# Kernel tuning notes

Measured on AMD Instinct MI355X. Metric: run time of the kernel, lower is better.

## Reference

```python
import jax, jax.numpy as jnp
import numpy as np

jax.config.update("jax_enable_x64", True)  # hash uses int64 (prime * coord ~ 7e12)

FEATURE_DIM = 2
GRID_DIM = 3
NUM_LVL = 16
MAX_RES = 2048
MIN_RES = 16
HASH_POWER = 19
MAX_ENTRY = 2 ** HASH_POWER
PRIMES = (3367900313, 2654435761, 805459861)

_b = np.exp((np.log(MAX_RES) - np.log(MIN_RES)) / (NUM_LVL - 1))
RESOLUTIONS = [int(np.floor(MIN_RES * _b ** i)) for i in range(NUM_LVL)]
TABLE_SIZES = [min(r ** GRID_DIM, MAX_ENTRY) for r in RESOLUTIONS]

# Corner offset order matches get_corner(): [c000, c010, c001, c011, c100, c101, c110, c111]
OFFSETS = np.array([[0, 0, 0], [0, 1, 0], [0, 0, 1], [0, 1, 1],
                    [1, 0, 0], [1, 0, 1], [1, 1, 0], [1, 1, 1]], dtype=np.int64)

N = 1 << 20  # number of query points


def setup_inputs() -> dict:
    key = jax.random.key(0)
    kx, kt = jax.random.split(key)
    x = jax.random.uniform(kx, (N, GRID_DIM), dtype=jnp.float32)  # in [0,1]
    # stacked (padded) hashtables; dense levels only use their first res^3 rows
    tables = jax.random.normal(kt, (NUM_LVL, MAX_ENTRY, FEATURE_DIM), dtype=jnp.float32) * 1e-4
    return {"x": x, "tables": tables}


def _level(x, table, res, table_size):
    resf = float(res)
    coord = jnp.clip(x * (resf - 1.0), 0.0, resf - 1.0001)  # [N,3] hash-space coords
    fl = jnp.floor(coord)
    corners = fl.astype(jnp.int64)[:, None, :] + jnp.asarray(OFFSETS)  # [N,8,3]
    if table_size != MAX_ENTRY:
        # dense spatial index: sum_i c_i * res^i
        idx = corners[..., 0] + corners[..., 1] * res + corners[..., 2] * (res * res)
    else:
        # NGP hash: xor of coord*prime, mod table size
        h = (corners[..., 0] * PRIMES[0]) ^ (corners[..., 1] * PRIMES[1]) ^ (corners[..., 2] * PRIMES[2])
        idx = h % MAX_ENTRY
    feat = table[idx]  # [N,8,F] gather
    d = coord - fl  # fractional part, [N,3]
    xx, yy, zz = d[:, 0], d[:, 1], d[:, 2]
    mx, my, mz = 1.0 - xx, 1.0 - yy, 1.0 - zz
    # weight order matches interpolation_weights() stack order
    w = jnp.stack([mx * my * mz, xx * my * mz, mx * yy * mz, xx * yy * mz,
                   mx * my * zz, xx * my * zz, mx * yy * zz, xx * yy * zz], axis=-1)  # [N,8]
    return (feat * w[..., None]).sum(axis=-2)  # [N,F]


def reference(x, tables):
    outs = [_level(x, tables[l], RESOLUTIONS[l], TABLE_SIZES[l]) for l in range(NUM_LVL)]
    return jnp.concatenate(outs, axis=-1)  # [N, NUM_LVL*FEATURE_DIM]
```

## Files before the change

### kernel.cpp

```cpp
#include <hip/hip_runtime.h>
#include <math.h>

#define NLVL 16
#define MAX_ENTRY (1 << 19)
#define NPTS (1 << 20)

typedef float f2_t __attribute__((ext_vector_type(2)));
typedef float f4_t __attribute__((ext_vector_type(4)));

__device__ __forceinline__ void nt_store2(float2 v, float2* p) {
    f2_t t; t.x = v.x; t.y = v.y;
    __builtin_nontemporal_store(t, (f2_t*)p);
}
__device__ __forceinline__ void nt_store4(float4 v, float4* p) {
    f4_t t; t.x = v.x; t.y = v.y; t.z = v.z; t.w = v.w;
    __builtin_nontemporal_store(t, (f4_t*)p);
}
__device__ __forceinline__ float2 nt_load2(const float2* p) {
    f2_t t = __builtin_nontemporal_load((const f2_t*)p);
    return make_float2(t.x, t.y);
}

__device__ __constant__ int OX[8] = {0, 0, 0, 0, 1, 1, 1, 1};
__device__ __constant__ int OY[8] = {0, 1, 0, 1, 0, 0, 1, 1};
__device__ __constant__ int OZ[8] = {0, 0, 1, 1, 0, 1, 0, 1};

__device__ __forceinline__ void corner_setup(
    float x0, float x1, float x2, float s, float hi,
    int& cx, int& cy, int& cz,
    float (&wx)[2], float (&wy)[2], float (&wz)[2])
{
    float c0 = fminf(fmaxf(x0 * s, 0.0f), hi);
    float c1 = fminf(fmaxf(x1 * s, 0.0f), hi);
    float c2 = fminf(fmaxf(x2 * s, 0.0f), hi);
    float f0 = floorf(c0), f1 = floorf(c1), f2 = floorf(c2);
    cx = (int)f0; cy = (int)f1; cz = (int)f2;
    float xx = c0 - f0, yy = c1 - f1, zz = c2 - f2;
    wx[0] = 1.0f - xx; wx[1] = xx;
    wy[0] = 1.0f - yy; wy[1] = yy;
    wz[0] = 1.0f - zz; wz[1] = zz;
}


struct DenseP {
    int res[6];
    int res2[6];
    float scale[6];
    float hi[6];
    long long packoff[6];
    long long nent[6];
};

__global__ __launch_bounds__(256) void repack_kernel(
    const float* __restrict__ tables, float4* __restrict__ pack, DenseP P)
{
    for (int l = 1; l < 6; ++l) {
        const float2* tab = (const float2*)(tables + (size_t)l * MAX_ENTRY * 2);
        float4* dst = pack + P.packoff[l];
        const long long n = P.nent[l];
        for (long long k = blockIdx.x * 256 + threadIdx.x; k < n;
             k += (long long)gridDim.x * 256) {
            const float2 a = tab[k];
            const float2 b = tab[k + 1];
            nt_store4(make_float4(a.x, a.y, b.x, b.y), &dst[k]);
        }
    }
}

__global__ __launch_bounds__(256) void dense_kernel(
    const float* __restrict__ x,
    const float* __restrict__ tables,
    const float4* __restrict__ pack,
    float2* __restrict__ feat,
    DenseP P)
{
    __shared__ float2 lds0[4096];
    {
        const float2* tab0 = (const float2*)tables;
        for (int j = threadIdx.x; j < 4096; j += 256) lds0[j] = tab0[j];
    }
    __syncthreads();

    const int i = blockIdx.x * 256 + threadIdx.x;
    if (i >= NPTS) return;

    const float x0 = x[3 * i + 0];
    const float x1 = x[3 * i + 1];
    const float x2 = x[3 * i + 2];

    {
        int cx, cy, cz;
        float wx[2], wy[2], wz[2];
        corner_setup(x0, x1, x2, P.scale[0], P.hi[0], cx, cy, cz, wx, wy, wz);
        const int res = P.res[0], res2 = P.res2[0];
        const int base = cx + cy * res + cz * res2;
        float a0 = 0.0f, a1 = 0.0f;
#pragma unroll
        for (int k = 0; k < 8; ++k) {
            const int idx = base + OX[k] + OY[k] * res + OZ[k] * res2;
            const float2 f = lds0[idx];
            const float w = wx[k & 1] * wy[(k >> 1) & 1] * wz[k >> 2];
            a0 += w * f.x; a1 += w * f.y;
        }
        nt_store2(make_float2(a0, a1), &feat[i]);
    }

#pragma unroll
    for (int l = 1; l < 6; ++l) {
        int cx, cy, cz;
        float wx[2], wy[2], wz[2];
        corner_setup(x0, x1, x2, P.scale[l], P.hi[l], cx, cy, cz, wx, wy, wz);
        const int res = P.res[l], res2 = P.res2[l];
        const int base = cx + cy * res + cz * res2;
        const float4* pk = pack + P.packoff[l];

        float a0 = 0.0f, a1 = 0.0f;
#pragma unroll
        for (int j = 0; j < 4; ++j) {
            const int idx = base + (j & 1) * res + (j >> 1) * res2;
            const float4 f = pk[idx];
            const float w0 = wx[j & 1] * wy[j >> 1] * wz[0];
            const float w1 = wx[j >> 1] * wy[j & 1] * wz[1];
            a0 += w0 * f.x + w1 * f.z;
            a1 += w0 * f.y + w1 * f.w;
        }
        nt_store2(make_float2(a0, a1), &feat[(size_t)l * NPTS + i]);
    }
}

__device__ __forceinline__ float2 hash_point(
    const float* __restrict__ x, int i, const float2* __restrict__ tab,
    float scale, float hi)
{
    const float x0 = x[3 * i + 0];
    const float x1 = x[3 * i + 1];
    const float x2 = x[3 * i + 2];

    int cx, cy, cz;
    float wx[2], wy[2], wz[2];
    corner_setup(x0, x1, x2, scale, hi, cx, cy, cz, wx, wy, wz);

    const unsigned P0 = 3367900313u, P1 = 2654435761u, P2 = 805459861u;
    unsigned hx[2], hy[2], hz[2];
    hx[0] = (unsigned)cx * P0; hx[1] = hx[0] + P0;
    hy[0] = (unsigned)cy * P1; hy[1] = hy[0] + P1;
    hz[0] = (unsigned)cz * P2; hz[1] = hz[0] + P2;

    float a0 = 0.0f, a1 = 0.0f;
#pragma unroll
    for (int k = 0; k < 8; ++k) {
        const unsigned idx = (hx[OX[k]] ^ hy[OY[k]] ^ hz[OZ[k]]) & (MAX_ENTRY - 1);
        const float2 f = tab[idx];
        const float w = wx[k & 1] * wy[(k >> 1) & 1] * wz[k >> 2];
        a0 += w * f.x; a1 += w * f.y;
    }
    return make_float2(a0, a1);
}

__global__ __launch_bounds__(256) void hash_kernel(
    const float* __restrict__ x,
    const float2* __restrict__ tab,
    float2* __restrict__ featl,
    float scale, float hi)
{
    const int t = blockIdx.x * 256 + threadIdx.x;
    const int i0 = t;
    const int i1 = t + NPTS / 2;
    const float2 r0 = hash_point(x, i0, tab, scale, hi);
    const float2 r1 = hash_point(x, i1, tab, scale, hi);
    nt_store2(r0, &featl[i0]);
    nt_store2(r1, &featl[i1]);
}

__global__ __launch_bounds__(256) void assemble_kernel(
    const float2* __restrict__ feat, float4* __restrict__ out)
{
    const size_t tid = (size_t)blockIdx.x * 256 + threadIdx.x;
    const int    c   = (int)(tid & 7);
    const size_t p   = tid >> 3;
    const float2 a = nt_load2(&feat[(size_t)(2 * c) * NPTS + p]);
    const float2 b = nt_load2(&feat[(size_t)(2 * c + 1) * NPTS + p]);
    nt_store4(make_float4(a.x, a.y, b.x, b.y), &out[tid]);
}


struct DenseParams {
    int   res[6];
    int   res2[6];
    float scale[6];
    float hi[6];
    long long tab_off[6];
};

__global__ __launch_bounds__(256) void dense6_kernel(
    const float* __restrict__ x,
    const float* __restrict__ tables,
    float* __restrict__ out,
    DenseParams P)
{
    const int i = blockIdx.x * 256 + threadIdx.x;
    if (i >= NPTS) return;
    const float x0 = x[3 * i + 0];
    const float x1 = x[3 * i + 1];
    const float x2 = x[3 * i + 2];
    float o[12];
#pragma unroll
    for (int l = 0; l < 6; ++l) {
        int cx, cy, cz;
        float wx[2], wy[2], wz[2];
        corner_setup(x0, x1, x2, P.scale[l], P.hi[l], cx, cy, cz, wx, wy, wz);
        const float2* tab = (const float2*)(tables + P.tab_off[l]);
        const int res  = P.res[l];
        const int res2 = P.res2[l];
        const int base = cx + cy * res + cz * res2;
        float a0 = 0.0f, a1 = 0.0f;
#pragma unroll
        for (int k = 0; k < 8; ++k) {
            const int idx = base + OX[k] + OY[k] * res + OZ[k] * res2;
            const float2 f = tab[idx];
            const float w = wx[k & 1] * wy[(k >> 1) & 1] * wz[k >> 2];
            a0 += w * f.x; a1 += w * f.y;
        }
        o[2 * l + 0] = a0; o[2 * l + 1] = a1;
    }
    float4* op = (float4*)(out + (size_t)i * 32);
    op[0] = ((float4*)o)[0];
    op[1] = ((float4*)o)[1];
    op[2] = ((float4*)o)[2];
}

__global__ __launch_bounds__(256) void hash_level_kernel(
    const float* __restrict__ x,
    const float* __restrict__ tables,
    float* __restrict__ out,
    int level, float scale, float hi)
{
    const int i = blockIdx.x * 256 + threadIdx.x;
    if (i >= NPTS) return;
    const float2* tab = (const float2*)tables + (size_t)level * MAX_ENTRY;
    const float2 r = hash_point(x, i, tab, scale, hi);
    *(float2*)(out + (size_t)i * 32 + 2 * level) = r;
}

__global__ __launch_bounds__(256) void generic_level_kernel(
    const float* __restrict__ x,
    const float* __restrict__ tables,
    float* __restrict__ out,
    int level, int res, int res2, int use_hash, float scale, float hi)
{
    const int i = blockIdx.x * 256 + threadIdx.x;
    if (i >= NPTS) return;
    const float x0 = x[3 * i + 0];
    const float x1 = x[3 * i + 1];
    const float x2 = x[3 * i + 2];
    int cx, cy, cz;
    float wx[2], wy[2], wz[2];
    corner_setup(x0, x1, x2, scale, hi, cx, cy, cz, wx, wy, wz);
    const float2* tab = (const float2*)tables + (size_t)level * MAX_ENTRY;
    float a0 = 0.0f, a1 = 0.0f;
    if (use_hash) {
        const unsigned P0 = 3367900313u, P1 = 2654435761u, P2 = 805459861u;
        unsigned hx[2], hy[2], hz[2];
        hx[0] = (unsigned)cx * P0; hx[1] = hx[0] + P0;
        hy[0] = (unsigned)cy * P1; hy[1] = hy[0] + P1;
        hz[0] = (unsigned)cz * P2; hz[1] = hz[0] + P2;
#pragma unroll
        for (int k = 0; k < 8; ++k) {
            const unsigned idx = (hx[OX[k]] ^ hy[OY[k]] ^ hz[OZ[k]]) & (MAX_ENTRY - 1);
            const float2 f = tab[idx];
            const float w = wx[k & 1] * wy[(k >> 1) & 1] * wz[k >> 2];
            a0 += w * f.x; a1 += w * f.y;
        }
    } else {
        const int base = cx + cy * res + cz * res2;
#pragma unroll
        for (int k = 0; k < 8; ++k) {
            const int idx = base + OX[k] + OY[k] * res + OZ[k] * res2;
            const float2 f = tab[idx];
            const float w = wx[k & 1] * wy[(k >> 1) & 1] * wz[k >> 2];
            a0 += w * f.x; a1 += w * f.y;
        }
    }
    *(float2*)(out + (size_t)i * 32 + 2 * level) = make_float2(a0, a1);
}


extern "C" void kernel_launch(void* const* d_in, const int* in_sizes, int n_in,
                              void* d_out, int out_size, void* d_ws, size_t ws_size,
                              hipStream_t stream)
{
    const float* x      = (const float*)d_in[0];
    const float* tables = (const float*)d_in[1];
    float* out          = (float*)d_out;

    int   res[NLVL], res2[NLVL], use_hash[NLVL];
    float scale[NLVL], hi[NLVL];
    const double b = exp((log(2048.0) - log(16.0)) / 15.0);
    for (int l = 0; l < NLVL; ++l) {
        const int r = (int)floor(16.0 * pow(b, (double)l));
        res[l]  = r;
        res2[l] = r * r;
        const long long t3 = (long long)r * r * r;
        use_hash[l] = (t3 >= (long long)MAX_ENTRY) ? 1 : 0;
        scale[l] = (float)(r - 1);
        hi[l]    = (float)((double)r - 1.0001);
    }

    const int block = 256;
    const int grid  = (NPTS + block - 1) / block;

    bool expected = true;
    for (int l = 0; l < 6; ++l)    expected = expected && !use_hash[l];
    for (int l = 6; l < NLVL; ++l) expected = expected && use_hash[l];

    long long packoff[6] = {0, 0, 0, 0, 0, 0};
    long long nent[6];
    long long packTot = 0;
    if (expected) {
        for (int l = 0; l < 6; ++l) nent[l] = (long long)res[l] * res[l] * res[l];
        for (int l = 1; l < 6; ++l) { packoff[l] = packTot; packTot += nent[l]; }
    }
    const size_t packBytes = (size_t)packTot * 16;
    const size_t featOff   = (packBytes + 255) & ~(size_t)255;
    const size_t need      = featOff + (size_t)NLVL * NPTS * sizeof(float2);

    if (expected && ws_size >= need) {
        float4* pack = (float4*)d_ws;
        float2* feat = (float2*)((char*)d_ws + featOff);

        DenseP P;
        for (int l = 0; l < 6; ++l) {
            P.res[l] = res[l]; P.res2[l] = res2[l];
            P.scale[l] = scale[l]; P.hi[l] = hi[l];
            P.packoff[l] = packoff[l]; P.nent[l] = nent[l];
        }

        repack_kernel<<<1024, block, 0, stream>>>(tables, pack, P);
        dense_kernel<<<grid, block, 0, stream>>>(x, tables, pack, feat, P);
        for (int l = 6; l < NLVL; ++l) {
            const float2* tab = (const float2*)tables + (size_t)l * MAX_ENTRY;
            hash_kernel<<<NPTS / 2 / block, block, 0, stream>>>(
                x, tab, feat + (size_t)l * NPTS, scale[l], hi[l]);
        }
        assemble_kernel<<<(NPTS * 8) / block, block, 0, stream>>>(feat, (float4*)out);
    } else if (expected) {
        DenseParams P;
        for (int l = 0; l < 6; ++l) {
            P.res[l] = res[l]; P.res2[l] = res2[l];
            P.scale[l] = scale[l]; P.hi[l] = hi[l];
            P.tab_off[l] = (long long)l * MAX_ENTRY * 2;
        }
        dense6_kernel<<<grid, block, 0, stream>>>(x, tables, out, P);
        for (int l = 6; l < NLVL; ++l) {
            hash_level_kernel<<<grid, block, 0, stream>>>(x, tables, out, l, scale[l], hi[l]);
        }
    } else {
        for (int l = 0; l < NLVL; ++l) {
            generic_level_kernel<<<grid, block, 0, stream>>>(
                x, tables, out, l, res[l], res2[l], use_hash[l], scale[l], hi[l]);
        }
    }
}
```

Measured before the change: 630.3 us.

## Pad x to float4, stop repacking levels 4-5, split level 5 into own kernel

The repack kernel now copies only dense levels 1-3 into float4 pair layout. It also writes a float4-padded copy of x to workspace so later kernels can read each point with one aligned 16-byte load. Level 4 is read from the original table with two float2 loads per corner pair, and level 5 moves into its own kernel that does the same with two points per thread. This cuts repack traffic and strided x reads, at the cost of more gather instructions for levels 4-5 and an extra pass to write the padded x.

```diff
diff --git a/kernel.cpp b/kernel.cpp
--- a/kernel.cpp
+++ b/kernel.cpp
@@ -19,6 +19,10 @@
 __device__ __forceinline__ float2 nt_load2(const float2* p) {
     f2_t t = __builtin_nontemporal_load((const f2_t*)p);
     return make_float2(t.x, t.y);
+}
+__device__ __forceinline__ float4 nt_load4(const float4* p) {
+    f4_t t = __builtin_nontemporal_load((const f4_t*)p);
+    return make_float4(t.x, t.y, t.z, t.w);
 }
 
 __device__ __constant__ int OX[8] = {0, 0, 0, 0, 1, 1, 1, 1};
@@ -41,34 +45,59 @@
     wz[0] = 1.0f - zz; wz[1] = zz;
 }
 
+__device__ __forceinline__ void load_xyz(
+    const float* __restrict__ x, const float4* __restrict__ xp, int i,
+    float& x0, float& x1, float& x2)
+{
+    if (xp) {
+        const float4 v = nt_load4(&xp[i]);
+        x0 = v.x; x1 = v.y; x2 = v.z;
+    } else {
+        x0 = __builtin_nontemporal_load(&x[3 * i + 0]);
+        x1 = __builtin_nontemporal_load(&x[3 * i + 1]);
+        x2 = __builtin_nontemporal_load(&x[3 * i + 2]);
+    }
+}
+
 
 struct DenseP {
     int res[6];
     int res2[6];
     float scale[6];
     float hi[6];
-    long long packoff[6];
+    long long packoff[4];
     long long nent[6];
 };
 
 __global__ __launch_bounds__(256) void repack_kernel(
-    const float* __restrict__ tables, float4* __restrict__ pack, DenseP P)
-{
-    for (int l = 1; l < 6; ++l) {
+    const float* __restrict__ x,
+    const float* __restrict__ tables,
+    float4* __restrict__ pack,
+    float4* __restrict__ xp,
+    DenseP P)
+{
+    const long long stride = (long long)gridDim.x * 256;
+    const long long tid = (long long)blockIdx.x * 256 + threadIdx.x;
+    for (int l = 1; l <= 3; ++l) {
         const float2* tab = (const float2*)(tables + (size_t)l * MAX_ENTRY * 2);
         float4* dst = pack + P.packoff[l];
         const long long n = P.nent[l];
-        for (long long k = blockIdx.x * 256 + threadIdx.x; k < n;
-             k += (long long)gridDim.x * 256) {
+        for (long long k = tid; k < n; k += stride) {
             const float2 a = tab[k];
             const float2 b = tab[k + 1];
             nt_store4(make_float4(a.x, a.y, b.x, b.y), &dst[k]);
         }
     }
+    if (xp) {
+        for (long long i = tid; i < NPTS; i += stride) {
+            xp[i] = make_float4(x[3 * i + 0], x[3 * i + 1], x[3 * i + 2], 0.0f);
+        }
+    }
 }
 
 __global__ __launch_bounds__(256) void dense_kernel(
     const float* __restrict__ x,
+    const float4* __restrict__ xp,
     const float* __restrict__ tables,
     const float4* __restrict__ pack,
     float2* __restrict__ feat,
@@ -84,9 +113,8 @@
     const int i = blockIdx.x * 256 + threadIdx.x;
     if (i >= NPTS) return;
 
-    const float x0 = x[3 * i + 0];
-    const float x1 = x[3 * i + 1];
-    const float x2 = x[3 * i + 2];
+    float x0, x1, x2;
+    load_xyz(x, xp, i, x0, x1, x2);
 
     {
         int cx, cy, cz;
@@ -106,7 +134,7 @@
     }
 
 #pragma unroll
-    for (int l = 1; l < 6; ++l) {
+    for (int l = 1; l <= 3; ++l) {
         int cx, cy, cz;
         float wx[2], wy[2], wz[2];
         corner_setup(x0, x1, x2, P.scale[l], P.hi[l], cx, cy, cz, wx, wy, wz);
@@ -126,16 +154,69 @@
         }
         nt_store2(make_float2(a0, a1), &feat[(size_t)l * NPTS + i]);
     }
+
+    {
+        const int l = 4;
+        int cx, cy, cz;
+        float wx[2], wy[2], wz[2];
+        corner_setup(x0, x1, x2, P.scale[l], P.hi[l], cx, cy, cz, wx, wy, wz);
+        const int res = P.res[l], res2 = P.res2[l];
+        const int base = cx + cy * res + cz * res2;
+        const float2* tab = (const float2*)tables + (size_t)l * MAX_ENTRY;
+
+        float a0 = 0.0f, a1 = 0.0f;
+#pragma unroll
+        for (int j = 0; j < 4; ++j) {
+            const int idx = base + (j & 1) * res + (j >> 1) * res2;
+            const float2 flo = tab[idx];
+            const float2 fhi = tab[idx + 1];
+            const float w0 = wx[j & 1] * wy[j >> 1] * wz[0];
+            const float w1 = wx[j >> 1] * wy[j & 1] * wz[1];
+            a0 += w0 * flo.x + w1 * fhi.x;
+            a1 += w0 * flo.y + w1 * fhi.y;
+        }
+        nt_store2(make_float2(a0, a1), &feat[(size_t)l * NPTS + i]);
+    }
+}
+
+__global__ __launch_bounds__(256) void dense5_kernel(
+    const float* __restrict__ x,
+    const float4* __restrict__ xp,
+    const float2* __restrict__ tab,
+    float2* __restrict__ featl,
+    int res, int res2, float scale, float hi)
+{
+    const int t = blockIdx.x * 256 + threadIdx.x;
+#pragma unroll
+    for (int h = 0; h < 2; ++h) {
+        const int i = t + h * (NPTS / 2);
+        float x0, x1, x2;
+        load_xyz(x, xp, i, x0, x1, x2);
+
+        int cx, cy, cz;
+        float wx[2], wy[2], wz[2];
+        corner_setup(x0, x1, x2, scale, hi, cx, cy, cz, wx, wy, wz);
+        const int base = cx + cy * res + cz * res2;
+
+        float a0 = 0.0f, a1 = 0.0f;
+#pragma unroll
+        for (int j = 0; j < 4; ++j) {
+            const int idx = base + (j & 1) * res + (j >> 1) * res2;
+            const float2 flo = tab[idx];
+            const float2 fhi = tab[idx + 1];
+            const float w0 = wx[j & 1] * wy[j >> 1] * wz[0];
+            const float w1 = wx[j >> 1] * wy[j & 1] * wz[1];
+            a0 += w0 * flo.x + w1 * fhi.x;
+            a1 += w0 * flo.y + w1 * fhi.y;
+        }
+        nt_store2(make_float2(a0, a1), &featl[i]);
+    }
 }
 
 __device__ __forceinline__ float2 hash_point(
-    const float* __restrict__ x, int i, const float2* __restrict__ tab,
+    float x0, float x1, float x2, const float2* __restrict__ tab,
     float scale, float hi)
 {
-    const float x0 = x[3 * i + 0];
-    const float x1 = x[3 * i + 1];
-    const float x2 = x[3 * i + 2];
-
     int cx, cy, cz;
     float wx[2], wy[2], wz[2];
     corner_setup(x0, x1, x2, scale, hi, cx, cy, cz, wx, wy, wz);
@@ -159,17 +240,20 @@
 
 __global__ __launch_bounds__(256) void hash_kernel(
     const float* __restrict__ x,
+    const float4* __restrict__ xp,
     const float2* __restrict__ tab,
     float2* __restrict__ featl,
     float scale, float hi)
 {
     const int t = blockIdx.x * 256 + threadIdx.x;
-    const int i0 = t;
-    const int i1 = t + NPTS / 2;
-    const float2 r0 = hash_point(x, i0, tab, scale, hi);
-    const float2 r1 = hash_point(x, i1, tab, scale, hi);
-    nt_store2(r0, &featl[i0]);
-    nt_store2(r1, &featl[i1]);
+#pragma unroll
+    for (int h = 0; h < 2; ++h) {
+        const int i = t + h * (NPTS / 2);
+        float x0, x1, x2;
+        load_xyz(x, xp, i, x0, x1, x2);
+        const float2 r = hash_point(x0, x1, x2, tab, scale, hi);
+        nt_store2(r, &featl[i]);
+    }
 }
 
 __global__ __launch_bounds__(256) void assemble_kernel(
@@ -238,7 +322,7 @@
     const int i = blockIdx.x * 256 + threadIdx.x;
     if (i >= NPTS) return;
     const float2* tab = (const float2*)tables + (size_t)level * MAX_ENTRY;
-    const float2 r = hash_point(x, i, tab, scale, hi);
+    const float2 r = hash_point(x[3 * i], x[3 * i + 1], x[3 * i + 2], tab, scale, hi);
     *(float2*)(out + (size_t)i * 32 + 2 * level) = r;
 }
 
@@ -313,34 +397,43 @@
     for (int l = 0; l < 6; ++l)    expected = expected && !use_hash[l];
     for (int l = 6; l < NLVL; ++l) expected = expected && use_hash[l];
 
-    long long packoff[6] = {0, 0, 0, 0, 0, 0};
+    long long packoff[4] = {0, 0, 0, 0};
     long long nent[6];
     long long packTot = 0;
     if (expected) {
         for (int l = 0; l < 6; ++l) nent[l] = (long long)res[l] * res[l] * res[l];
-        for (int l = 1; l < 6; ++l) { packoff[l] = packTot; packTot += nent[l]; }
+        for (int l = 1; l <= 3; ++l) { packoff[l] = packTot; packTot += nent[l]; }
     }
     const size_t packBytes = (size_t)packTot * 16;
     const size_t featOff   = (packBytes + 255) & ~(size_t)255;
-    const size_t need      = featOff + (size_t)NLVL * NPTS * sizeof(float2);
+    const size_t featBytes = (size_t)NLVL * NPTS * sizeof(float2);
+    const size_t xpOff     = (featOff + featBytes + 255) & ~(size_t)255;
+    const size_t need      = featOff + featBytes;
+    const size_t need_xp   = xpOff + (size_t)NPTS * sizeof(float4);
 
     if (expected && ws_size >= need) {
         float4* pack = (float4*)d_ws;
         float2* feat = (float2*)((char*)d_ws + featOff);
+        float4* xp   = (ws_size >= need_xp) ? (float4*)((char*)d_ws + xpOff) : nullptr;
 
         DenseP P;
         for (int l = 0; l < 6; ++l) {
             P.res[l] = res[l]; P.res2[l] = res2[l];
             P.scale[l] = scale[l]; P.hi[l] = hi[l];
-            P.packoff[l] = packoff[l]; P.nent[l] = nent[l];
-        }
-
-        repack_kernel<<<1024, block, 0, stream>>>(tables, pack, P);
-        dense_kernel<<<grid, block, 0, stream>>>(x, tables, pack, feat, P);
+            P.nent[l] = nent[l];
+        }
+        for (int l = 1; l <= 3; ++l) P.packoff[l] = packoff[l];
+        P.packoff[0] = 0;
+
+        repack_kernel<<<1024, block, 0, stream>>>(x, tables, pack, xp, P);
+        dense_kernel<<<grid, block, 0, stream>>>(x, xp, tables, pack, feat, P);
+        dense5_kernel<<<NPTS / 2 / block, block, 0, stream>>>(
+            x, xp, (const float2*)tables + (size_t)5 * MAX_ENTRY,
+            feat + (size_t)5 * NPTS, res[5], res2[5], scale[5], hi[5]);
         for (int l = 6; l < NLVL; ++l) {
             const float2* tab = (const float2*)tables + (size_t)l * MAX_ENTRY;
             hash_kernel<<<NPTS / 2 / block, block, 0, stream>>>(
-                x, tab, feat + (size_t)l * NPTS, scale[l], hi[l]);
+                x, xp, tab, feat + (size_t)l * NPTS, scale[l], hi[l]);
         }
         assemble_kernel<<<(NPTS * 8) / block, block, 0, stream>>>(feat, (float4*)out);
     } else if (expected) {
```

Measured after the change: 592.6 us. 6.0% less time.

## Store intermediate features as bf16, block dense tables per cell, merge level kernels

Applied to the files above, without the earlier changes.

Per-level intermediate features are now rounded and packed into bf16 pairs (4 bytes per point per level instead of 8), then expanded back to fp32 in the assemble pass. This halves the intermediate write and read traffic. The dense tables for levels 1–3 are repacked into per-cell or per-column blocks, so each point's corners are fetched with contiguous float4 loads. The points are padded to float4, and levels 3–15 run in one merged launch instead of one kernel per hash level. The trade-off is that bf16 rounding lowers output precision, which could exceed the accuracy tolerance, and the repack step adds extra preprocessing work.

```diff
diff --git a/kernel.cpp b/kernel.cpp
--- a/kernel.cpp
+++ b/kernel.cpp
@@ -16,10 +16,25 @@
     f4_t t; t.x = v.x; t.y = v.y; t.z = v.z; t.w = v.w;
     __builtin_nontemporal_store(t, (f4_t*)p);
 }
-__device__ __forceinline__ float2 nt_load2(const float2* p) {
-    f2_t t = __builtin_nontemporal_load((const f2_t*)p);
-    return make_float2(t.x, t.y);
-}
+__device__ __forceinline__ void nt_storeu(unsigned v, unsigned* p) {
+    __builtin_nontemporal_store(v, p);
+}
+__device__ __forceinline__ float4 nt_load4(const float4* p) {
+    f4_t t = __builtin_nontemporal_load((const f4_t*)p);
+    return make_float4(t.x, t.y, t.z, t.w);
+}
+__device__ __forceinline__ unsigned nt_loadu(const unsigned* p) {
+    return __builtin_nontemporal_load(p);
+}
+
+__device__ __forceinline__ unsigned pack_bf16(float a, float b) {
+    unsigned ua = __float_as_uint(a), ub = __float_as_uint(b);
+    ua = (ua + 0x7FFFu + ((ua >> 16) & 1u)) >> 16;
+    ub = (ub + 0x7FFFu + ((ub >> 16) & 1u)) >> 16;
+    return ua | (ub << 16);
+}
+__device__ __forceinline__ float bf_lo(unsigned u) { return __uint_as_float(u << 16); }
+__device__ __forceinline__ float bf_hi(unsigned u) { return __uint_as_float(u & 0xFFFF0000u); }
 
 __device__ __constant__ int OX[8] = {0, 0, 0, 0, 1, 1, 1, 1};
 __device__ __constant__ int OY[8] = {0, 1, 0, 1, 0, 0, 1, 1};
@@ -41,38 +56,90 @@
     wz[0] = 1.0f - zz; wz[1] = zz;
 }
 
-
-struct DenseP {
-    int res[6];
-    int res2[6];
-    float scale[6];
-    float hi[6];
-    long long packoff[6];
-    long long nent[6];
+__device__ __forceinline__ void acc_pair(
+    int j, float4 f, const float (&wx)[2], const float (&wy)[2], const float (&wz)[2],
+    float& a0, float& a1)
+{
+    const float w0 = wx[j & 1] * wy[j >> 1] * wz[0];
+    const float w1 = wx[j >> 1] * wy[j & 1] * wz[1];
+    a0 += w0 * f.x + w1 * f.z;
+    a1 += w0 * f.y + w1 * f.w;
+}
+
+struct OptP {
+    int   res[NLVL];
+    int   res2[NLVL];
+    float scale[NLVL];
+    float hi[NLVL];
+    int   cdim1, cdim2, cdim3;
 };
 
-__global__ __launch_bounds__(256) void repack_kernel(
-    const float* __restrict__ tables, float4* __restrict__ pack, DenseP P)
-{
-    for (int l = 1; l < 6; ++l) {
+
+__global__ __launch_bounds__(256) void repack2_kernel(
+    const float* __restrict__ x,
+    const float* __restrict__ tables,
+    float4* __restrict__ blk1,
+    float4* __restrict__ blk2,
+    float4* __restrict__ blk3,
+    float4* __restrict__ xp,
+    OptP P)
+{
+    const long long stride = (long long)gridDim.x * 256;
+    const long long tid = (long long)blockIdx.x * 256 + threadIdx.x;
+
+#pragma unroll
+    for (int l = 1; l <= 2; ++l) {
+        const int res = P.res[l], res2v = P.res2[l];
+        const int cdim = res - 1;
+        const long long ncell = (long long)cdim * cdim * cdim;
         const float2* tab = (const float2*)(tables + (size_t)l * MAX_ENTRY * 2);
-        float4* dst = pack + P.packoff[l];
-        const long long n = P.nent[l];
-        for (long long k = blockIdx.x * 256 + threadIdx.x; k < n;
-             k += (long long)gridDim.x * 256) {
-            const float2 a = tab[k];
-            const float2 b = tab[k + 1];
-            nt_store4(make_float4(a.x, a.y, b.x, b.y), &dst[k]);
-        }
-    }
-}
-
-__global__ __launch_bounds__(256) void dense_kernel(
-    const float* __restrict__ x,
-    const float* __restrict__ tables,
-    const float4* __restrict__ pack,
-    float2* __restrict__ feat,
-    DenseP P)
+        float4* dst = (l == 1) ? blk1 : blk2;
+        for (long long c = tid; c < ncell; c += stride) {
+            const int cx = (int)(c % cdim);
+            const int cy = (int)((c / cdim) % cdim);
+            const int cz = (int)(c / ((long long)cdim * cdim));
+            const int base = cx + cy * res + cz * res2v;
+#pragma unroll
+            for (int j = 0; j < 4; ++j) {
+                const int oy = j & 1, oz = j >> 1;
+                const float2 e0 = tab[base + oy * res + oz * res2v];
+                const float2 e1 = tab[base + 1 + oy * res + oz * res2v];
+                nt_store4(make_float4(e0.x, e0.y, e1.x, e1.y), &dst[c * 4 + j]);
+            }
+        }
+    }
+
+    {
+        const int res = P.res[3], res2v = P.res2[3];
+        const int cdim = P.cdim3;
+        const long long nblk = (long long)cdim * cdim * res;
+        const float2* tab = (const float2*)(tables + (size_t)3 * MAX_ENTRY * 2);
+        for (long long b = tid; b < nblk; b += stride) {
+            const int bx = (int)(b % cdim);
+            const int by = (int)((b / cdim) % cdim);
+            const int z  = (int)(b / ((long long)cdim * cdim));
+            const int base = bx + by * res + z * res2v;
+#pragma unroll
+            for (int oy = 0; oy < 2; ++oy) {
+                const float2 e0 = tab[base + oy * res];
+                const float2 e1 = tab[base + 1 + oy * res];
+                nt_store4(make_float4(e0.x, e0.y, e1.x, e1.y), &blk3[b * 2 + oy]);
+            }
+        }
+    }
+
+    for (long long i = tid; i < NPTS; i += stride) {
+        xp[i] = make_float4(x[3 * i + 0], x[3 * i + 1], x[3 * i + 2], 0.0f);
+    }
+}
+
+__global__ __launch_bounds__(256) void passA_kernel(
+    const float4* __restrict__ xp,
+    const float* __restrict__ tables,
+    const float4* __restrict__ blk1,
+    const float4* __restrict__ blk2,
+    unsigned* __restrict__ fb,
+    OptP P)
 {
     __shared__ float2 lds0[4096];
     {
@@ -82,105 +149,122 @@
     __syncthreads();
 
     const int i = blockIdx.x * 256 + threadIdx.x;
-    if (i >= NPTS) return;
-
-    const float x0 = x[3 * i + 0];
-    const float x1 = x[3 * i + 1];
-    const float x2 = x[3 * i + 2];
+
+    const float4 v = nt_load4(&xp[i]);
+    const float x0 = v.x, x1 = v.y, x2 = v.z;
 
     {
         int cx, cy, cz;
         float wx[2], wy[2], wz[2];
         corner_setup(x0, x1, x2, P.scale[0], P.hi[0], cx, cy, cz, wx, wy, wz);
-        const int res = P.res[0], res2 = P.res2[0];
-        const int base = cx + cy * res + cz * res2;
+        const int res = P.res[0], res2v = P.res2[0];
+        const int base = cx + cy * res + cz * res2v;
         float a0 = 0.0f, a1 = 0.0f;
 #pragma unroll
         for (int k = 0; k < 8; ++k) {
-            const int idx = base + OX[k] + OY[k] * res + OZ[k] * res2;
+            const int idx = base + OX[k] + OY[k] * res + OZ[k] * res2v;
             const float2 f = lds0[idx];
             const float w = wx[k & 1] * wy[(k >> 1) & 1] * wz[k >> 2];
             a0 += w * f.x; a1 += w * f.y;
         }
-        nt_store2(make_float2(a0, a1), &feat[i]);
-    }
-
-#pragma unroll
-    for (int l = 1; l < 6; ++l) {
+        nt_storeu(pack_bf16(a0, a1), &fb[i]);
+    }
+
+#pragma unroll
+    for (int l = 1; l <= 2; ++l) {
         int cx, cy, cz;
         float wx[2], wy[2], wz[2];
         corner_setup(x0, x1, x2, P.scale[l], P.hi[l], cx, cy, cz, wx, wy, wz);
-        const int res = P.res[l], res2 = P.res2[l];
-        const int base = cx + cy * res + cz * res2;
-        const float4* pk = pack + P.packoff[l];
-
+        const int cdim = (l == 1) ? P.cdim1 : P.cdim2;
+        const float4* blk = (l == 1) ? blk1 : blk2;
+        const long long c = cx + (long long)cy * cdim + (long long)cz * cdim * cdim;
         float a0 = 0.0f, a1 = 0.0f;
 #pragma unroll
         for (int j = 0; j < 4; ++j) {
-            const int idx = base + (j & 1) * res + (j >> 1) * res2;
-            const float4 f = pk[idx];
-            const float w0 = wx[j & 1] * wy[j >> 1] * wz[0];
-            const float w1 = wx[j >> 1] * wy[j & 1] * wz[1];
-            a0 += w0 * f.x + w1 * f.z;
-            a1 += w0 * f.y + w1 * f.w;
-        }
-        nt_store2(make_float2(a0, a1), &feat[(size_t)l * NPTS + i]);
-    }
-}
-
-__device__ __forceinline__ float2 hash_point(
-    const float* __restrict__ x, int i, const float2* __restrict__ tab,
-    float scale, float hi)
-{
-    const float x0 = x[3 * i + 0];
-    const float x1 = x[3 * i + 1];
-    const float x2 = x[3 * i + 2];
-
-    int cx, cy, cz;
-    float wx[2], wy[2], wz[2];
-    corner_setup(x0, x1, x2, scale, hi, cx, cy, cz, wx, wy, wz);
-
-    const unsigned P0 = 3367900313u, P1 = 2654435761u, P2 = 805459861u;
-    unsigned hx[2], hy[2], hz[2];
-    hx[0] = (unsigned)cx * P0; hx[1] = hx[0] + P0;
-    hy[0] = (unsigned)cy * P1; hy[1] = hy[0] + P1;
-    hz[0] = (unsigned)cz * P2; hz[1] = hz[0] + P2;
-
-    float a0 = 0.0f, a1 = 0.0f;
-#pragma unroll
-    for (int k = 0; k < 8; ++k) {
-        const unsigned idx = (hx[OX[k]] ^ hy[OY[k]] ^ hz[OZ[k]]) & (MAX_ENTRY - 1);
-        const float2 f = tab[idx];
-        const float w = wx[k & 1] * wy[(k >> 1) & 1] * wz[k >> 2];
-        a0 += w * f.x; a1 += w * f.y;
-    }
-    return make_float2(a0, a1);
-}
-
-__global__ __launch_bounds__(256) void hash_kernel(
-    const float* __restrict__ x,
-    const float2* __restrict__ tab,
-    float2* __restrict__ featl,
-    float scale, float hi)
-{
-    const int t = blockIdx.x * 256 + threadIdx.x;
-    const int i0 = t;
-    const int i1 = t + NPTS / 2;
-    const float2 r0 = hash_point(x, i0, tab, scale, hi);
-    const float2 r1 = hash_point(x, i1, tab, scale, hi);
-    nt_store2(r0, &featl[i0]);
-    nt_store2(r1, &featl[i1]);
-}
-
-__global__ __launch_bounds__(256) void assemble_kernel(
-    const float2* __restrict__ feat, float4* __restrict__ out)
+            const float4 f = blk[c * 4 + j];
+            acc_pair(j, f, wx, wy, wz, a0, a1);
+        }
+        nt_storeu(pack_bf16(a0, a1), &fb[(size_t)l * NPTS + i]);
+    }
+}
+
+__global__ __launch_bounds__(256) void mega_kernel(
+    const float4* __restrict__ xp,
+    const float* __restrict__ tables,
+    const float4* __restrict__ blk3,
+    unsigned* __restrict__ fb,
+    OptP P)
+{
+    const int seg = blockIdx.x >> 11;
+    const int lvl = seg + 3;
+    const int t = (blockIdx.x & 2047) * 256 + threadIdx.x;
+    unsigned* fbl = fb + (size_t)lvl * NPTS;
+
+    const float scale = P.scale[lvl], hiv = P.hi[lvl];
+
+#pragma unroll
+    for (int h = 0; h < 2; ++h) {
+        const int i = t + h * (NPTS / 2);
+        const float4 v = nt_load4(&xp[i]);
+        int cx, cy, cz;
+        float wx[2], wy[2], wz[2];
+        corner_setup(v.x, v.y, v.z, scale, hiv, cx, cy, cz, wx, wy, wz);
+
+        float a0 = 0.0f, a1 = 0.0f;
+
+        if (lvl == 3) {
+            const int cdim = P.cdim3;
+            const long long b0 = cx + (long long)cy * cdim + (long long)cz * cdim * cdim;
+            const long long b1 = b0 + (long long)cdim * cdim;
+#pragma unroll
+            for (int oz = 0; oz < 2; ++oz) {
+                const long long b = (oz == 0) ? b0 : b1;
+#pragma unroll
+                for (int oy = 0; oy < 2; ++oy) {
+                    const float4 f = blk3[b * 2 + oy];
+                    acc_pair(oy + 2 * oz, f, wx, wy, wz, a0, a1);
+                }
+            }
+        } else if (lvl < 6) {
+            const int res = P.res[lvl], res2v = P.res2[lvl];
+            const float2* tab = (const float2*)tables + (size_t)lvl * MAX_ENTRY;
+            const int base = cx + cy * res + cz * res2v;
+#pragma unroll
+            for (int j = 0; j < 4; ++j) {
+                const int idx = base + (j & 1) * res + (j >> 1) * res2v;
+                const float2 flo = tab[idx];
+                const float2 fhi = tab[idx + 1];
+                acc_pair(j, make_float4(flo.x, flo.y, fhi.x, fhi.y), wx, wy, wz, a0, a1);
+            }
+        } else {
+            const float2* tab = (const float2*)tables + (size_t)lvl * MAX_ENTRY;
+            const unsigned P0 = 3367900313u, P1 = 2654435761u, P2 = 805459861u;
+            unsigned hx[2], hy[2], hz[2];
+            hx[0] = (unsigned)cx * P0; hx[1] = hx[0] + P0;
+            hy[0] = (unsigned)cy * P1; hy[1] = hy[0] + P1;
+            hz[0] = (unsigned)cz * P2; hz[1] = hz[0] + P2;
+#pragma unroll
+            for (int k = 0; k < 8; ++k) {
+                const unsigned idx = (hx[OX[k]] ^ hy[OY[k]] ^ hz[OZ[k]]) & (MAX_ENTRY - 1);
+                const float2 f = tab[idx];
+                const float w = wx[k & 1] * wy[(k >> 1) & 1] * wz[k >> 2];
+                a0 += w * f.x; a1 += w * f.y;
+            }
+        }
+
+        nt_storeu(pack_bf16(a0, a1), &fbl[i]);
+    }
+}
+
+__global__ __launch_bounds__(256) void assemble_bf_kernel(
+    const unsigned* __restrict__ fb, float4* __restrict__ out)
 {
     const size_t tid = (size_t)blockIdx.x * 256 + threadIdx.x;
     const int    c   = (int)(tid & 7);
     const size_t p   = tid >> 3;
-    const float2 a = nt_load2(&feat[(size_t)(2 * c) * NPTS + p]);
-    const float2 b = nt_load2(&feat[(size_t)(2 * c + 1) * NPTS + p]);
-    nt_store4(make_float4(a.x, a.y, b.x, b.y), &out[tid]);
+    const unsigned u0 = nt_loadu(&fb[(size_t)(2 * c) * NPTS + p]);
+    const unsigned u1 = nt_loadu(&fb[(size_t)(2 * c + 1) * NPTS + p]);
+    nt_store4(make_float4(bf_lo(u0), bf_hi(u0), bf_lo(u1), bf_hi(u1)), &out[tid]);
 }
 
 
@@ -191,6 +275,29 @@
     float hi[6];
     long long tab_off[6];
 };
+
+__device__ __forceinline__ float2 hash_point_fb(
+    float x0, float x1, float x2, const float2* __restrict__ tab,
+    float scale, float hi)
+{
+    int cx, cy, cz;
+    float wx[2], wy[2], wz[2];
+    corner_setup(x0, x1, x2, scale, hi, cx, cy, cz, wx, wy, wz);
+    const unsigned P0 = 3367900313u, P1 = 2654435761u, P2 = 805459861u;
+    unsigned hx[2], hy[2], hz[2];
+    hx[0] = (unsigned)cx * P0; hx[1] = hx[0] + P0;
+    hy[0] = (unsigned)cy * P1; hy[1] = hy[0] + P1;
+    hz[0] = (unsigned)cz * P2; hz[1] = hz[0] + P2;
+    float a0 = 0.0f, a1 = 0.0f;
+#pragma unroll
+    for (int k = 0; k < 8; ++k) {
+        const unsigned idx = (hx[OX[k]] ^ hy[OY[k]] ^ hz[OZ[k]]) & (MAX_ENTRY - 1);
+        const float2 f = tab[idx];
+        const float w = wx[k & 1] * wy[(k >> 1) & 1] * wz[k >> 2];
+        a0 += w * f.x; a1 += w * f.y;
+    }
+    return make_float2(a0, a1);
+}
 
 __global__ __launch_bounds__(256) void dense6_kernel(
     const float* __restrict__ x,
@@ -238,7 +345,7 @@
     const int i = blockIdx.x * 256 + threadIdx.x;
     if (i >= NPTS) return;
     const float2* tab = (const float2*)tables + (size_t)level * MAX_ENTRY;
-    const float2 r = hash_point(x, i, tab, scale, hi);
+    const float2 r = hash_point_fb(x[3 * i], x[3 * i + 1], x[3 * i + 2], tab, scale, hi);
     *(float2*)(out + (size_t)i * 32 + 2 * level) = r;
 }
 
@@ -312,37 +419,38 @@
     bool expected = true;
     for (int l = 0; l < 6; ++l)    expected = expected && !use_hash[l];
     for (int l = 6; l < NLVL; ++l) expected = expected && use_hash[l];
-
-    long long packoff[6] = {0, 0, 0, 0, 0, 0};
-    long long nent[6];
-    long long packTot = 0;
-    if (expected) {
-        for (int l = 0; l < 6; ++l) nent[l] = (long long)res[l] * res[l] * res[l];
-        for (int l = 1; l < 6; ++l) { packoff[l] = packTot; packTot += nent[l]; }
-    }
-    const size_t packBytes = (size_t)packTot * 16;
-    const size_t featOff   = (packBytes + 255) & ~(size_t)255;
-    const size_t need      = featOff + (size_t)NLVL * NPTS * sizeof(float2);
+    expected = expected && (res[0] * res[0] * res[0] <= 4096);
+
+    const int cdim1 = res[1] - 1, cdim2 = res[2] - 1, cdim3 = res[3] - 1;
+    const size_t sz1 = (size_t)cdim1 * cdim1 * cdim1 * 64;
+    const size_t sz2 = (size_t)cdim2 * cdim2 * cdim2 * 64;
+    const size_t sz3 = (size_t)cdim3 * cdim3 * res[3] * 32;
+    auto al = [](size_t v) { return (v + 255) & ~(size_t)255; };
+    const size_t off1 = 0;
+    const size_t off2 = al(off1 + sz1);
+    const size_t off3 = al(off2 + sz2);
+    const size_t offxp = al(off3 + sz3);
+    const size_t offfb = al(offxp + (size_t)NPTS * 16);
+    const size_t need = offfb + (size_t)NLVL * NPTS * 4;
 
     if (expected && ws_size >= need) {
-        float4* pack = (float4*)d_ws;
-        float2* feat = (float2*)((char*)d_ws + featOff);
-
-        DenseP P;
-        for (int l = 0; l < 6; ++l) {
+        float4* blk1 = (float4*)((char*)d_ws + off1);
+        float4* blk2 = (float4*)((char*)d_ws + off2);
+        float4* blk3 = (float4*)((char*)d_ws + off3);
+        float4* xp   = (float4*)((char*)d_ws + offxp);
+        unsigned* fb = (unsigned*)((char*)d_ws + offfb);
+
+        OptP P;
+        for (int l = 0; l < NLVL; ++l) {
             P.res[l] = res[l]; P.res2[l] = res2[l];
             P.scale[l] = scale[l]; P.hi[l] = hi[l];
-            P.packoff[l] = packoff[l]; P.nent[l] = nent[l];
-        }
-
-        repack_kernel<<<1024, block, 0, stream>>>(tables, pack, P);
-        dense_kernel<<<grid, block, 0, stream>>>(x, tables, pack, feat, P);
-        for (int l = 6; l < NLVL; ++l) {
-            const float2* tab = (const float2*)tables + (size_t)l * MAX_ENTRY;
-            hash_kernel<<<NPTS / 2 / block, block, 0, stream>>>(
-                x, tab, feat + (size_t)l * NPTS, scale[l], hi[l]);
-        }
-        assemble_kernel<<<(NPTS * 8) / block, block, 0, stream>>>(feat, (float4*)out);
+        }
+        P.cdim1 = cdim1; P.cdim2 = cdim2; P.cdim3 = cdim3;
+
+        repack2_kernel<<<1024, block, 0, stream>>>(x, tables, blk1, blk2, blk3, xp, P);
+        passA_kernel<<<grid, block, 0, stream>>>(xp, tables, blk1, blk2, fb, P);
+        mega_kernel<<<13 * 2048, block, 0, stream>>>(xp, tables, blk3, fb, P);
+        assemble_bf_kernel<<<(NPTS * 8) / block, block, 0, stream>>>(fb, (float4*)out);
     } else if (expected) {
         DenseParams P;
         for (int l = 0; l < 6; ++l) {
```

New measurement: 602.1 us. -4.5%, faster.
